# Optimization experiments

Measured on AMD Instinct MI355X. Metric: run time of the kernel, lower is better.

## Reference

```python
import jax, jax.numpy as jnp
import numpy as np

N = 100000      # num nodes
E = 1600000     # num edges
F_IN = 602      # Reddit input features
H = 256         # num_hidden
C = 42          # num_classes


def gcn_conv(x, src, dst, W, b, num_nodes):
    """PyG GCNConv: add self loops, symmetric deg^-1/2 normalization, scatter-add."""
    h = x @ W  # [N, out] dense transform first (PyG order)
    self_idx = jnp.arange(num_nodes, dtype=src.dtype)
    s = jnp.concatenate([src, self_idx])  # [E+N]
    d = jnp.concatenate([dst, self_idx])
    deg = jax.ops.segment_sum(jnp.ones_like(d, dtype=h.dtype), d, num_segments=num_nodes)
    dinv = deg ** -0.5  # deg >= 1 due to self loops
    norm = dinv[s] * dinv[d]  # [E+N]
    msg = h[s] * norm[:, None]  # [E+N, out] gather + scale
    out = jax.ops.segment_sum(msg, d, num_segments=num_nodes)  # scatter-add
    return out + b


def setup_inputs() -> dict:
    key = jax.random.key(0)
    k = jax.random.split(key, 5)
    x = jax.random.normal(k[0], (N, F_IN), dtype=jnp.float32)
    edge_index = jax.random.randint(k[1], (2, E), 0, N, dtype=jnp.int32)
    # Glorot-style init for GCNConv linear weights; bias zeros (PyG default)
    W1 = jax.random.normal(k[2], (F_IN, H), dtype=jnp.float32) * np.float32(1.0 / np.sqrt(F_IN))
    b1 = jnp.zeros((H,), dtype=jnp.float32)
    W2 = jax.random.normal(k[3], (H, C), dtype=jnp.float32) * np.float32(1.0 / np.sqrt(H))
    b2 = jnp.zeros((C,), dtype=jnp.float32)
    return {"x": x, "edge_index": edge_index, "W1": W1, "b1": b1, "W2": W2, "b2": b2}


def reference(x, edge_index, W1, b1, W2, b2):
    src, dst = edge_index[0], edge_index[1]
    num_nodes = x.shape[0]
    h = gcn_conv(x, src, dst, W1, b1, num_nodes)
    h = jax.nn.relu(h)
    # dropout is identity in eval mode (deterministic reference)
    out = gcn_conv(h, src, dst, W2, b2, num_nodes)
    return jax.nn.log_softmax(out, axis=1)
```

## Files before the change

### kernel.cpp

```cpp
#include <hip/hip_runtime.h>
#include <stdint.h>

#define NN 100000
#define NE 1600000
#define FIN 602
#define KP1 608
#define H 256
#define C 42
#define NP2 48
#define NB1 98

typedef __bf16 bf16;
typedef __bf16 bf16x8 __attribute__((ext_vector_type(8)));
typedef float f32x4 __attribute__((ext_vector_type(4)));

__device__ __forceinline__ float b2f(bf16 v) { return (float)v; }
__device__ __forceinline__ bf16 f2b(float v) { return (bf16)v; }
__device__ __forceinline__ float us2f(unsigned short u) {
    union { unsigned int i; float f; } w; w.i = ((unsigned int)u) << 16; return w.f;
}


__global__ void k_zero(int* __restrict__ p, int n) {
    int i = blockIdx.x * 256 + threadIdx.x;
    if (i < n) p[i] = 0;
}

__global__ void k_count(const int* __restrict__ dst, int* __restrict__ cnt) {
    int e = blockIdx.x * 256 + threadIdx.x;
    if (e < NE) atomicAdd(&cnt[dst[e]], 1);
}

__global__ void k_dinv(const int* __restrict__ cnt, float* __restrict__ dinv) {
    int i = blockIdx.x * 256 + threadIdx.x;
    if (i < NN) dinv[i] = rsqrtf((float)(cnt[i] + 1));
}

__global__ __launch_bounds__(256) void k_scan1(const int* __restrict__ cnt,
                                               int* __restrict__ excl, int* __restrict__ bsum) {
    __shared__ int ts[256];
    const int tid = threadIdx.x;
    const int base = blockIdx.x * 1024 + tid * 4;
    int v[4];
#pragma unroll
    for (int j = 0; j < 4; ++j) v[j] = (base + j < NN) ? cnt[base + j] : 0;
    int s = v[0] + v[1] + v[2] + v[3];
    ts[tid] = s;
    __syncthreads();
    for (int off = 1; off < 256; off <<= 1) {
        int t = (tid >= off) ? ts[tid - off] : 0;
        __syncthreads();
        if (tid >= off) ts[tid] += t;
        __syncthreads();
    }
    int prefix = ts[tid] - s;
    if (tid == 255) bsum[blockIdx.x] = ts[255];
    int run = prefix;
#pragma unroll
    for (int j = 0; j < 4; ++j) {
        if (base + j < NN) excl[base + j] = run;
        run += v[j];
    }
}

__global__ __launch_bounds__(128) void k_scan2(int* __restrict__ bsum) {
    __shared__ int ts[128];
    const int tid = threadIdx.x;
    int v = (tid < NB1) ? bsum[tid] : 0;
    ts[tid] = v;
    __syncthreads();
    for (int off = 1; off < 128; off <<= 1) {
        int t = (tid >= off) ? ts[tid - off] : 0;
        __syncthreads();
        if (tid >= off) ts[tid] += t;
        __syncthreads();
    }
    if (tid < NB1) bsum[tid] = ts[tid] - v;
}

__global__ __launch_bounds__(256) void k_scan3(const int* __restrict__ excl, const int* __restrict__ bsum,
                                               int* __restrict__ rowptr, int* __restrict__ cursor) {
    const int tid = threadIdx.x;
    const int base = blockIdx.x * 1024 + tid * 4;
    const int add = bsum[blockIdx.x];
#pragma unroll
    for (int j = 0; j < 4; ++j) {
        int i = base + j;
        if (i < NN) { int r = excl[i] + add; rowptr[i] = r; cursor[i] = r; }
    }
    if (blockIdx.x == 0 && tid == 0) rowptr[NN] = NE;
}

__global__ void k_fill(const int* __restrict__ src, const int* __restrict__ dst,
                       int* __restrict__ cursor, int* __restrict__ esrc) {
    int e = blockIdx.x * 256 + threadIdx.x;
    if (e < NE) {
        int d = dst[e];
        int pos = atomicAdd(&cursor[d], 1);
        esrc[pos] = src[e];
    }
}


__global__ void k_transpose_w1(const float* __restrict__ w1, bf16* __restrict__ w1t) {
    int idx = blockIdx.x * 256 + threadIdx.x;
    int n = idx / KP1;
    int k = idx % KP1;
    w1t[idx] = (k < FIN) ? f2b(w1[(size_t)k * H + n]) : (bf16)0.0f;
}

__global__ void k_transpose_w2(const float* __restrict__ w2, bf16* __restrict__ w2t) {
    int idx = blockIdx.x * 256 + threadIdx.x;
    int n = idx >> 8;
    int k = idx & 255;
    w2t[idx] = (n < C) ? f2b(w2[(size_t)k * C + n]) : (bf16)0.0f;
}


__global__ __launch_bounds__(256) void k_gemm1(const float* __restrict__ x,
                                               const bf16* __restrict__ w1t,
                                               bf16* __restrict__ h1) {
    __shared__ bf16 As[64 * 32];
    const int tid = threadIdx.x;
    const int wave = tid >> 6;
    const int lane = tid & 63;
    const int q = lane >> 4;
    const int r = lane & 15;
    const int row0 = blockIdx.x * 64;

    const int srow = tid >> 2;
    const int sseg = tid & 3;
    int gsrow = row0 + srow;
    if (gsrow >= NN) gsrow = NN - 1;
    const float* xrow = x + (size_t)gsrow * FIN + sseg * 8;

    f32x4 acc[4][4];
#pragma unroll
    for (int a = 0; a < 4; ++a)
#pragma unroll
        for (int b = 0; b < 4; ++b) acc[a][b] = (f32x4){0.f, 0.f, 0.f, 0.f};

    const bf16* bbase = w1t + (size_t)(wave * 64) * KP1;

    for (int kk = 0; kk < 19; ++kk) {
        const int k0 = kk * 32;
        const int c0 = k0 + sseg * 8;
        union { bf16 s[8]; uint4 u; } pk;
        if (c0 + 8 <= FIN) {
            const float2* p = (const float2*)(xrow + k0);
            float2 f0 = p[0], f1 = p[1], f2 = p[2], f3 = p[3];
            pk.s[0] = f2b(f0.x); pk.s[1] = f2b(f0.y);
            pk.s[2] = f2b(f1.x); pk.s[3] = f2b(f1.y);
            pk.s[4] = f2b(f2.x); pk.s[5] = f2b(f2.y);
            pk.s[6] = f2b(f3.x); pk.s[7] = f2b(f3.y);
        } else {
#pragma unroll
            for (int j = 0; j < 8; ++j)
                pk.s[j] = (c0 + j < FIN) ? f2b(xrow[k0 + j]) : (bf16)0.0f;
        }
        __syncthreads();
        *(uint4*)(As + srow * 32 + sseg * 8) = pk.u;
        __syncthreads();

        bf16x8 af[4];
#pragma unroll
        for (int rt = 0; rt < 4; ++rt) {
            union { uint4 u; bf16x8 v; } ua;
            ua.u = *(const uint4*)(As + (rt * 16 + r) * 32 + q * 8);
            af[rt] = ua.v;
        }
#pragma unroll
        for (int ct = 0; ct < 4; ++ct) {
            const bf16* bp = bbase + (size_t)(ct * 16 + r) * KP1 + k0 + q * 8;
            union { uint4 u; bf16x8 v; } ub;
            ub.u = *(const uint4*)bp;
#pragma unroll
            for (int rt = 0; rt < 4; ++rt)
                acc[rt][ct] = __builtin_amdgcn_mfma_f32_16x16x32_bf16(af[rt], ub.v, acc[rt][ct], 0, 0, 0);
        }
    }

#pragma unroll
    for (int rt = 0; rt < 4; ++rt) {
#pragma unroll
        for (int ct = 0; ct < 4; ++ct) {
            const int col = wave * 64 + ct * 16 + r;
#pragma unroll
            for (int rr = 0; rr < 4; ++rr) {
                const int m = row0 + rt * 16 + q * 4 + rr;
                if (m < NN) h1[(size_t)m * H + col] = f2b(acc[rt][ct][rr]);
            }
        }
    }
}


__global__ __launch_bounds__(64) void k_gather1(const int* __restrict__ rowptr,
                                                const int* __restrict__ esrc,
                                                const bf16* __restrict__ h1,
                                                const float* __restrict__ dinv,
                                                const float* __restrict__ b1,
                                                bf16* __restrict__ hb) {
    const int n = blockIdx.x;
    const int tid = threadIdx.x;
    const float dn = dinv[n];

    uint2 u = ((const uint2*)(h1 + (size_t)n * H))[tid];
    float ws = dn * dn;
    float a0 = us2f((unsigned short)(u.x & 0xffff)) * ws;
    float a1 = us2f((unsigned short)(u.x >> 16)) * ws;
    float a2 = us2f((unsigned short)(u.y & 0xffff)) * ws;
    float a3 = us2f((unsigned short)(u.y >> 16)) * ws;

    const int beg = rowptr[n], end = rowptr[n + 1];
    int j = beg;
    for (; j + 3 < end; j += 4) {
        int s0 = esrc[j], s1 = esrc[j + 1], s2 = esrc[j + 2], s3 = esrc[j + 3];
        float w0 = dinv[s0] * dn, w1 = dinv[s1] * dn, w2 = dinv[s2] * dn, w3 = dinv[s3] * dn;
        uint2 v0 = ((const uint2*)(h1 + (size_t)s0 * H))[tid];
        uint2 v1 = ((const uint2*)(h1 + (size_t)s1 * H))[tid];
        uint2 v2 = ((const uint2*)(h1 + (size_t)s2 * H))[tid];
        uint2 v3 = ((const uint2*)(h1 + (size_t)s3 * H))[tid];
        a0 += us2f((unsigned short)(v0.x & 0xffff)) * w0;
        a1 += us2f((unsigned short)(v0.x >> 16)) * w0;
        a2 += us2f((unsigned short)(v0.y & 0xffff)) * w0;
        a3 += us2f((unsigned short)(v0.y >> 16)) * w0;
        a0 += us2f((unsigned short)(v1.x & 0xffff)) * w1;
        a1 += us2f((unsigned short)(v1.x >> 16)) * w1;
        a2 += us2f((unsigned short)(v1.y & 0xffff)) * w1;
        a3 += us2f((unsigned short)(v1.y >> 16)) * w1;
        a0 += us2f((unsigned short)(v2.x & 0xffff)) * w2;
        a1 += us2f((unsigned short)(v2.x >> 16)) * w2;
        a2 += us2f((unsigned short)(v2.y & 0xffff)) * w2;
        a3 += us2f((unsigned short)(v2.y >> 16)) * w2;
        a0 += us2f((unsigned short)(v3.x & 0xffff)) * w3;
        a1 += us2f((unsigned short)(v3.x >> 16)) * w3;
        a2 += us2f((unsigned short)(v3.y & 0xffff)) * w3;
        a3 += us2f((unsigned short)(v3.y >> 16)) * w3;
    }
    for (; j < end; ++j) {
        int s = esrc[j];
        float w = dinv[s] * dn;
        uint2 v = ((const uint2*)(h1 + (size_t)s * H))[tid];
        a0 += us2f((unsigned short)(v.x & 0xffff)) * w;
        a1 += us2f((unsigned short)(v.x >> 16)) * w;
        a2 += us2f((unsigned short)(v.y & 0xffff)) * w;
        a3 += us2f((unsigned short)(v.y >> 16)) * w;
    }

    float4 bb = ((const float4*)b1)[tid];
    a0 += bb.x; a1 += bb.y; a2 += bb.z; a3 += bb.w;
    a0 = a0 > 0.f ? a0 : 0.f;
    a1 = a1 > 0.f ? a1 : 0.f;
    a2 = a2 > 0.f ? a2 : 0.f;
    a3 = a3 > 0.f ? a3 : 0.f;

    union { unsigned short s[4]; uint2 u; } pk;
    union { bf16 b; unsigned short s; } cv;
    cv.b = f2b(a0); pk.s[0] = cv.s;
    cv.b = f2b(a1); pk.s[1] = cv.s;
    cv.b = f2b(a2); pk.s[2] = cv.s;
    cv.b = f2b(a3); pk.s[3] = cv.s;
    ((uint2*)(hb + (size_t)n * H))[tid] = pk.u;
}


__global__ __launch_bounds__(256) void k_gemm2(const bf16* __restrict__ hb,
                                               const bf16* __restrict__ w2t,
                                               bf16* __restrict__ h2) {
    __shared__ bf16 As[256 * 32];
    const int tid = threadIdx.x;
    const int wave = tid >> 6;
    const int lane = tid & 63;
    const int q = lane >> 4;
    const int r = lane & 15;
    const int row0 = blockIdx.x * 256;

    int gsrow = row0 + tid;
    if (gsrow >= NN) gsrow = NN - 1;
    const bf16* arow = hb + (size_t)gsrow * H;

    f32x4 acc[4][3];
#pragma unroll
    for (int a = 0; a < 4; ++a)
#pragma unroll
        for (int b = 0; b < 3; ++b) acc[a][b] = (f32x4){0.f, 0.f, 0.f, 0.f};

    for (int kk = 0; kk < 8; ++kk) {
        const int k0 = kk * 32;
        uint4 c0 = *(const uint4*)(arow + k0);
        uint4 c1 = *(const uint4*)(arow + k0 + 8);
        uint4 c2 = *(const uint4*)(arow + k0 + 16);
        uint4 c3 = *(const uint4*)(arow + k0 + 24);
        __syncthreads();
        uint4* ldst = (uint4*)(As + tid * 32);
        ldst[0] = c0; ldst[1] = c1; ldst[2] = c2; ldst[3] = c3;
        __syncthreads();

        bf16x8 af[4];
#pragma unroll
        for (int rt = 0; rt < 4; ++rt) {
            union { uint4 u; bf16x8 v; } ua;
            ua.u = *(const uint4*)(As + (wave * 64 + rt * 16 + r) * 32 + q * 8);
            af[rt] = ua.v;
        }
#pragma unroll
        for (int ct = 0; ct < 3; ++ct) {
            const bf16* bp = w2t + (size_t)(ct * 16 + r) * H + k0 + q * 8;
            union { uint4 u; bf16x8 v; } ub;
            ub.u = *(const uint4*)bp;
#pragma unroll
            for (int rt = 0; rt < 4; ++rt)
                acc[rt][ct] = __builtin_amdgcn_mfma_f32_16x16x32_bf16(af[rt], ub.v, acc[rt][ct], 0, 0, 0);
        }
    }

#pragma unroll
    for (int rt = 0; rt < 4; ++rt) {
#pragma unroll
        for (int ct = 0; ct < 3; ++ct) {
            const int col = ct * 16 + r;
            if (col < C) {
#pragma unroll
                for (int rr = 0; rr < 4; ++rr) {
                    const int m = row0 + wave * 64 + rt * 16 + q * 4 + rr;
                    if (m < NN) h2[(size_t)m * C + col] = f2b(acc[rt][ct][rr]);
                }
            }
        }
    }
}


__global__ __launch_bounds__(64) void k_gather2(const int* __restrict__ rowptr,
                                                const int* __restrict__ esrc,
                                                const bf16* __restrict__ h2,
                                                const float* __restrict__ dinv,
                                                const float* __restrict__ b2,
                                                float* __restrict__ out) {
    const int n = blockIdx.x;
    const int c = threadIdx.x;
    const float dn = dinv[n];

    float acc = 0.f;
    if (c < C) acc = b2f(h2[(size_t)n * C + c]) * dn * dn;

    const int beg = rowptr[n], end = rowptr[n + 1];
    int j = beg;
    for (; j + 3 < end; j += 4) {
        int s0 = esrc[j], s1 = esrc[j + 1], s2 = esrc[j + 2], s3 = esrc[j + 3];
        float w0 = dinv[s0] * dn, w1 = dinv[s1] * dn, w2 = dinv[s2] * dn, w3 = dinv[s3] * dn;
        if (c < C) {
            float v0 = b2f(h2[(size_t)s0 * C + c]);
            float v1 = b2f(h2[(size_t)s1 * C + c]);
            float v2 = b2f(h2[(size_t)s2 * C + c]);
            float v3 = b2f(h2[(size_t)s3 * C + c]);
            acc += v0 * w0 + v1 * w1 + v2 * w2 + v3 * w3;
        }
    }
    for (; j < end; ++j) {
        int s = esrc[j];
        float w = dinv[s] * dn;
        if (c < C) acc += b2f(h2[(size_t)s * C + c]) * w;
    }

    float v = (c < C) ? acc + b2[c] : -INFINITY;
    float m = v;
#pragma unroll
    for (int o = 32; o > 0; o >>= 1) m = fmaxf(m, __shfl_xor(m, o, 64));
    float ex = (c < C) ? expf(v - m) : 0.f;
    float s = ex;
#pragma unroll
    for (int o = 32; o > 0; o >>= 1) s += __shfl_xor(s, o, 64);
    if (c < C) out[(size_t)n * C + c] = (v - m) - logf(s);
}


extern "C" void kernel_launch(void* const* d_in, const int* in_sizes, int n_in,
                              void* d_out, int out_size, void* d_ws, size_t ws_size,
                              hipStream_t stream) {
    const float* x  = (const float*)d_in[0];
    const int*   ei = (const int*)d_in[1];
    const float* w1 = (const float*)d_in[2];
    const float* b1 = (const float*)d_in[3];
    const float* w2 = (const float*)d_in[4];
    const float* b2 = (const float*)d_in[5];
    float* out = (float*)d_out;

    const int* src = ei;
    const int* dst = ei + NE;

    char* base = (char*)d_ws;
    size_t off = 0;
    auto alloc = [&](size_t bytes) -> void* {
        void* p = base + off;
        off += (bytes + 255) & ~(size_t)255;
        return p;
    };
    int*   cnt    = (int*)alloc((size_t)NN * 4);
    float* dinv   = (float*)alloc((size_t)NN * 4);
    int*   excl   = (int*)alloc((size_t)NN * 4);
    int*   bsum   = (int*)alloc(128 * 4);
    int*   rowptr = (int*)alloc((size_t)(NN + 1) * 4);
    int*   cursor = (int*)alloc((size_t)NN * 4);
    int*   esrc   = (int*)alloc((size_t)NE * 4);
    bf16*  w1t    = (bf16*)alloc((size_t)H * KP1 * 2);
    bf16*  w2t    = (bf16*)alloc((size_t)NP2 * H * 2);
    bf16*  h1     = (bf16*)alloc((size_t)NN * H * 2);
    bf16*  hb     = (bf16*)alloc((size_t)NN * H * 2);
    bf16*  h2     = (bf16*)alloc((size_t)NN * C * 2);
    (void)ws_size;

    k_zero<<<dim3((NN + 255) / 256), dim3(256), 0, stream>>>(cnt, NN);
    k_count<<<dim3((NE + 255) / 256), dim3(256), 0, stream>>>(dst, cnt);
    k_dinv<<<dim3((NN + 255) / 256), dim3(256), 0, stream>>>(cnt, dinv);
    k_scan1<<<dim3(NB1), dim3(256), 0, stream>>>(cnt, excl, bsum);
    k_scan2<<<dim3(1), dim3(128), 0, stream>>>(bsum);
    k_scan3<<<dim3(NB1), dim3(256), 0, stream>>>(excl, bsum, rowptr, cursor);
    k_fill<<<dim3((NE + 255) / 256), dim3(256), 0, stream>>>(src, dst, cursor, esrc);

    k_transpose_w1<<<dim3(KP1), dim3(256), 0, stream>>>(w1, w1t);
    k_transpose_w2<<<dim3(NP2), dim3(256), 0, stream>>>(w2, w2t);

    k_gemm1<<<dim3((NN + 63) / 64), dim3(256), 0, stream>>>(x, w1t, h1);
    k_gather1<<<dim3(NN), dim3(64), 0, stream>>>(rowptr, esrc, h1, dinv, b1, hb);

    k_gemm2<<<dim3((NN + 255) / 256), dim3(256), 0, stream>>>(hb, w2t, h2);
    k_gather2<<<dim3(NN), dim3(64), 0, stream>>>(rowptr, esrc, h2, dinv, b2, out);
}
```

Measured before the change: 796.2 us.

## Double-buffer LDS tiles with register prefetch in both GEMM kernels

Both dense GEMM kernels now prefetch the next A tiles into registers two steps ahead and alternate between two padded LDS buffers, which cuts the barriers per k-step to one. LDS row stride is padded to 40 elements to reduce bank conflicts. k_gemm2 moves to 128-row tiles with more blocks. This is meant to hide global load latency behind MFMA work, at the cost of more registers and LDS per block.

```diff
diff --git a/kernel.cpp b/kernel.cpp
--- a/kernel.cpp
+++ b/kernel.cpp
@@ -9,6 +9,8 @@
 #define C 42
 #define NP2 48
 #define NB1 98
+#define LDA1 40
+#define LDA2 40
 
 typedef __bf16 bf16;
 typedef __bf16 bf16x8 __attribute__((ext_vector_type(8)));
@@ -117,10 +119,60 @@
 }
 
 
+__device__ __forceinline__ void g1_load(const float* xrow, int kk, int sseg, float2 rx[4]) {
+    const int k0 = kk * 32;
+    const int c0 = k0 + sseg * 8;
+    if (c0 + 8 <= FIN) {
+        const float2* p = (const float2*)(xrow + k0);
+        rx[0] = p[0]; rx[1] = p[1]; rx[2] = p[2]; rx[3] = p[3];
+    } else {
+        float t[8];
+#pragma unroll
+        for (int j = 0; j < 8; ++j) t[j] = (c0 + j < FIN) ? xrow[k0 + j] : 0.f;
+        rx[0] = make_float2(t[0], t[1]);
+        rx[1] = make_float2(t[2], t[3]);
+        rx[2] = make_float2(t[4], t[5]);
+        rx[3] = make_float2(t[6], t[7]);
+    }
+}
+
+__device__ __forceinline__ void g1_step(int kk, const float* xrow, float2 rx[4],
+                                        bf16* buf, int srow, int sseg, int q, int r,
+                                        const bf16* bbase, f32x4 acc[4][4], bool prefetch) {
+    union { bf16 s[8]; uint4 u; } pk;
+    pk.s[0] = f2b(rx[0].x); pk.s[1] = f2b(rx[0].y);
+    pk.s[2] = f2b(rx[1].x); pk.s[3] = f2b(rx[1].y);
+    pk.s[4] = f2b(rx[2].x); pk.s[5] = f2b(rx[2].y);
+    pk.s[6] = f2b(rx[3].x); pk.s[7] = f2b(rx[3].y);
+    *(uint4*)(buf + srow * LDA1 + sseg * 8) = pk.u;
+    if (prefetch) g1_load(xrow, kk + 2, sseg, rx);
+    asm volatile("s_waitcnt lgkmcnt(0)" ::: "memory");
+    __builtin_amdgcn_s_barrier();
+
+    const int k0 = kk * 32;
+    bf16x8 af[4];
+#pragma unroll
+    for (int rt = 0; rt < 4; ++rt) {
+        union { uint4 u; bf16x8 v; } ua;
+        ua.u = *(const uint4*)(buf + (rt * 16 + r) * LDA1 + q * 8);
+        af[rt] = ua.v;
+    }
+#pragma unroll
+    for (int ct = 0; ct < 4; ++ct) {
+        const bf16* bp = bbase + (size_t)(ct * 16 + r) * KP1 + k0 + q * 8;
+        union { uint4 u; bf16x8 v; } ub;
+        ub.u = *(const uint4*)bp;
+#pragma unroll
+        for (int rt = 0; rt < 4; ++rt)
+            acc[rt][ct] = __builtin_amdgcn_mfma_f32_16x16x32_bf16(af[rt], ub.v, acc[rt][ct], 0, 0, 0);
+    }
+}
+
 __global__ __launch_bounds__(256) void k_gemm1(const float* __restrict__ x,
                                                const bf16* __restrict__ w1t,
                                                bf16* __restrict__ h1) {
-    __shared__ bf16 As[64 * 32];
+    __shared__ bf16 As0[64 * LDA1];
+    __shared__ bf16 As1[64 * LDA1];
     const int tid = threadIdx.x;
     const int wave = tid >> 6;
     const int lane = tid & 63;
@@ -142,42 +194,15 @@
 
     const bf16* bbase = w1t + (size_t)(wave * 64) * KP1;
 
-    for (int kk = 0; kk < 19; ++kk) {
-        const int k0 = kk * 32;
-        const int c0 = k0 + sseg * 8;
-        union { bf16 s[8]; uint4 u; } pk;
-        if (c0 + 8 <= FIN) {
-            const float2* p = (const float2*)(xrow + k0);
-            float2 f0 = p[0], f1 = p[1], f2 = p[2], f3 = p[3];
-            pk.s[0] = f2b(f0.x); pk.s[1] = f2b(f0.y);
-            pk.s[2] = f2b(f1.x); pk.s[3] = f2b(f1.y);
-            pk.s[4] = f2b(f2.x); pk.s[5] = f2b(f2.y);
-            pk.s[6] = f2b(f3.x); pk.s[7] = f2b(f3.y);
-        } else {
-#pragma unroll
-            for (int j = 0; j < 8; ++j)
-                pk.s[j] = (c0 + j < FIN) ? f2b(xrow[k0 + j]) : (bf16)0.0f;
-        }
-        __syncthreads();
-        *(uint4*)(As + srow * 32 + sseg * 8) = pk.u;
-        __syncthreads();
-
-        bf16x8 af[4];
-#pragma unroll
-        for (int rt = 0; rt < 4; ++rt) {
-            union { uint4 u; bf16x8 v; } ua;
-            ua.u = *(const uint4*)(As + (rt * 16 + r) * 32 + q * 8);
-            af[rt] = ua.v;
-        }
-#pragma unroll
-        for (int ct = 0; ct < 4; ++ct) {
-            const bf16* bp = bbase + (size_t)(ct * 16 + r) * KP1 + k0 + q * 8;
-            union { uint4 u; bf16x8 v; } ub;
-            ub.u = *(const uint4*)bp;
-#pragma unroll
-            for (int rt = 0; rt < 4; ++rt)
-                acc[rt][ct] = __builtin_amdgcn_mfma_f32_16x16x32_bf16(af[rt], ub.v, acc[rt][ct], 0, 0, 0);
-        }
+    float2 ra[4], rb[4];
+    g1_load(xrow, 0, sseg, ra);
+    g1_load(xrow, 1, sseg, rb);
+
+#pragma unroll 1
+    for (int kk = 0; kk < 19; kk += 2) {
+        g1_step(kk, xrow, ra, As0, srow, sseg, q, r, bbase, acc, kk + 2 < 19);
+        if (kk + 1 < 19)
+            g1_step(kk + 1, xrow, rb, As1, srow, sseg, q, r, bbase, acc, kk + 3 < 19);
     }
 
 #pragma unroll
@@ -265,65 +290,83 @@
 }
 
 
+__device__ __forceinline__ void g2_load(const bf16* arow, int kk, uint4 rx[2]) {
+    const bf16* p = arow + kk * 32;
+    rx[0] = *(const uint4*)p;
+    rx[1] = *(const uint4*)(p + 8);
+}
+
+__device__ __forceinline__ void g2_step(int kk, const bf16* arow, uint4 rx[2],
+                                        bf16* buf, int srow, int sseg, int q, int r, int wave,
+                                        const bf16* w2t, f32x4 acc[2][3], bool prefetch) {
+    *(uint4*)(buf + srow * LDA2 + sseg * 16) = rx[0];
+    *(uint4*)(buf + srow * LDA2 + sseg * 16 + 8) = rx[1];
+    if (prefetch) g2_load(arow, kk + 2, rx);
+    asm volatile("s_waitcnt lgkmcnt(0)" ::: "memory");
+    __builtin_amdgcn_s_barrier();
+
+    const int k0 = kk * 32;
+    bf16x8 af[2];
+#pragma unroll
+    for (int rt = 0; rt < 2; ++rt) {
+        union { uint4 u; bf16x8 v; } ua;
+        ua.u = *(const uint4*)(buf + (wave * 32 + rt * 16 + r) * LDA2 + q * 8);
+        af[rt] = ua.v;
+    }
+#pragma unroll
+    for (int ct = 0; ct < 3; ++ct) {
+        const bf16* bp = w2t + (size_t)(ct * 16 + r) * H + k0 + q * 8;
+        union { uint4 u; bf16x8 v; } ub;
+        ub.u = *(const uint4*)bp;
+#pragma unroll
+        for (int rt = 0; rt < 2; ++rt)
+            acc[rt][ct] = __builtin_amdgcn_mfma_f32_16x16x32_bf16(af[rt], ub.v, acc[rt][ct], 0, 0, 0);
+    }
+}
+
 __global__ __launch_bounds__(256) void k_gemm2(const bf16* __restrict__ hb,
                                                const bf16* __restrict__ w2t,
                                                bf16* __restrict__ h2) {
-    __shared__ bf16 As[256 * 32];
+    __shared__ bf16 As0[128 * LDA2];
+    __shared__ bf16 As1[128 * LDA2];
     const int tid = threadIdx.x;
     const int wave = tid >> 6;
     const int lane = tid & 63;
     const int q = lane >> 4;
     const int r = lane & 15;
-    const int row0 = blockIdx.x * 256;
-
-    int gsrow = row0 + tid;
+    const int row0 = blockIdx.x * 128;
+
+    const int srow = tid >> 1;
+    const int sseg = tid & 1;
+    int gsrow = row0 + srow;
     if (gsrow >= NN) gsrow = NN - 1;
-    const bf16* arow = hb + (size_t)gsrow * H;
-
-    f32x4 acc[4][3];
-#pragma unroll
-    for (int a = 0; a < 4; ++a)
+    const bf16* arow = hb + (size_t)gsrow * H + sseg * 16;
+
+    f32x4 acc[2][3];
+#pragma unroll
+    for (int a = 0; a < 2; ++a)
 #pragma unroll
         for (int b = 0; b < 3; ++b) acc[a][b] = (f32x4){0.f, 0.f, 0.f, 0.f};
 
-    for (int kk = 0; kk < 8; ++kk) {
-        const int k0 = kk * 32;
-        uint4 c0 = *(const uint4*)(arow + k0);
-        uint4 c1 = *(const uint4*)(arow + k0 + 8);
-        uint4 c2 = *(const uint4*)(arow + k0 + 16);
-        uint4 c3 = *(const uint4*)(arow + k0 + 24);
-        __syncthreads();
-        uint4* ldst = (uint4*)(As + tid * 32);
-        ldst[0] = c0; ldst[1] = c1; ldst[2] = c2; ldst[3] = c3;
-        __syncthreads();
-
-        bf16x8 af[4];
-#pragma unroll
-        for (int rt = 0; rt < 4; ++rt) {
-            union { uint4 u; bf16x8 v; } ua;
-            ua.u = *(const uint4*)(As + (wave * 64 + rt * 16 + r) * 32 + q * 8);
-            af[rt] = ua.v;
-        }
-#pragma unroll
-        for (int ct = 0; ct < 3; ++ct) {
-            const bf16* bp = w2t + (size_t)(ct * 16 + r) * H + k0 + q * 8;
-            union { uint4 u; bf16x8 v; } ub;
-            ub.u = *(const uint4*)bp;
-#pragma unroll
-            for (int rt = 0; rt < 4; ++rt)
-                acc[rt][ct] = __builtin_amdgcn_mfma_f32_16x16x32_bf16(af[rt], ub.v, acc[rt][ct], 0, 0, 0);
-        }
-    }
-
-#pragma unroll
-    for (int rt = 0; rt < 4; ++rt) {
+    uint4 ra[2], rb[2];
+    g2_load(arow, 0, ra);
+    g2_load(arow, 1, rb);
+
+#pragma unroll 1
+    for (int kk = 0; kk < 8; kk += 2) {
+        g2_step(kk, arow, ra, As0, srow, sseg, q, r, wave, w2t, acc, kk + 2 < 8);
+        g2_step(kk + 1, arow, rb, As1, srow, sseg, q, r, wave, w2t, acc, kk + 3 < 8);
+    }
+
+#pragma unroll
+    for (int rt = 0; rt < 2; ++rt) {
 #pragma unroll
         for (int ct = 0; ct < 3; ++ct) {
             const int col = ct * 16 + r;
             if (col < C) {
 #pragma unroll
                 for (int rr = 0; rr < 4; ++rr) {
-                    const int m = row0 + wave * 64 + rt * 16 + q * 4 + rr;
+                    const int m = row0 + wave * 32 + rt * 16 + q * 4 + rr;
                     if (m < NN) h2[(size_t)m * C + col] = f2b(acc[rt][ct][rr]);
                 }
             }
@@ -425,6 +468,6 @@
     k_gemm1<<<dim3((NN + 63) / 64), dim3(256), 0, stream>>>(x, w1t, h1);
     k_gather1<<<dim3(NN), dim3(64), 0, stream>>>(rowptr, esrc, h1, dinv, b1, hb);
 
-    k_gemm2<<<dim3((NN + 255) / 256), dim3(256), 0, stream>>>(hb, w2t, h2);
+    k_gemm2<<<dim3((NN + 127) / 128), dim3(256), 0, stream>>>(hb, w2t, h2);
     k_gather2<<<dim3(NN), dim3(64), 0, stream>>>(rowptr, esrc, h2, dinv, b2, out);
 }
```

New measurement: 812.9 us. 2.1% more time.

## Load GEMM A fragments directly from global memory, dropping LDS staging and barriers

Applied to the files above, without the earlier changes.

Both dense GEMM kernels now read A-operand fragments straight from global memory into registers instead of staging tiles through shared memory with two barriers per k-step. gemm1 splits the 256 output columns across two blocks per row tile, and gemm2 uses smaller 128-row blocks, to raise block counts. The aim is to remove synchronization stalls and LDS traffic. In exchange, x rows are read redundantly by multiple waves and blocks and the global loads are less coalesced, so cache and bandwidth pressure goes up.

```diff
diff --git a/kernel.cpp b/kernel.cpp
--- a/kernel.cpp
+++ b/kernel.cpp
@@ -120,71 +120,94 @@
 __global__ __launch_bounds__(256) void k_gemm1(const float* __restrict__ x,
                                                const bf16* __restrict__ w1t,
                                                bf16* __restrict__ h1) {
-    __shared__ bf16 As[64 * 32];
     const int tid = threadIdx.x;
     const int wave = tid >> 6;
     const int lane = tid & 63;
     const int q = lane >> 4;
     const int r = lane & 15;
-    const int row0 = blockIdx.x * 64;
-
-    const int srow = tid >> 2;
-    const int sseg = tid & 3;
-    int gsrow = row0 + srow;
-    if (gsrow >= NN) gsrow = NN - 1;
-    const float* xrow = x + (size_t)gsrow * FIN + sseg * 8;
-
-    f32x4 acc[4][4];
+    const int b = blockIdx.x;
+    const int row0 = (b >> 1) * 64;
+    const int col0 = (b & 1) * 128 + wave * 32;
+
+    const float* arow[4];
+#pragma unroll
+    for (int rt = 0; rt < 4; ++rt) {
+        int m = row0 + rt * 16 + r;
+        if (m >= NN) m = NN - 1;
+        arow[rt] = x + (size_t)m * FIN + q * 8;
+    }
+    const bf16* brow[2];
+#pragma unroll
+    for (int ct = 0; ct < 2; ++ct)
+        brow[ct] = w1t + (size_t)(col0 + ct * 16 + r) * KP1 + q * 8;
+
+    f32x4 acc[4][2];
 #pragma unroll
     for (int a = 0; a < 4; ++a)
 #pragma unroll
-        for (int b = 0; b < 4; ++b) acc[a][b] = (f32x4){0.f, 0.f, 0.f, 0.f};
-
-    const bf16* bbase = w1t + (size_t)(wave * 64) * KP1;
-
-    for (int kk = 0; kk < 19; ++kk) {
+        for (int c = 0; c < 2; ++c) acc[a][c] = (f32x4){0.f, 0.f, 0.f, 0.f};
+
+#pragma unroll 2
+    for (int kk = 0; kk < 18; ++kk) {
         const int k0 = kk * 32;
-        const int c0 = k0 + sseg * 8;
-        union { bf16 s[8]; uint4 u; } pk;
-        if (c0 + 8 <= FIN) {
-            const float2* p = (const float2*)(xrow + k0);
+        bf16x8 af[4];
+#pragma unroll
+        for (int rt = 0; rt < 4; ++rt) {
+            const float2* p = (const float2*)(arow[rt] + k0);
             float2 f0 = p[0], f1 = p[1], f2 = p[2], f3 = p[3];
+            union { bf16 s[8]; bf16x8 v; } pk;
             pk.s[0] = f2b(f0.x); pk.s[1] = f2b(f0.y);
             pk.s[2] = f2b(f1.x); pk.s[3] = f2b(f1.y);
             pk.s[4] = f2b(f2.x); pk.s[5] = f2b(f2.y);
             pk.s[6] = f2b(f3.x); pk.s[7] = f2b(f3.y);
-        } else {
-#pragma unroll
-            for (int j = 0; j < 8; ++j)
-                pk.s[j] = (c0 + j < FIN) ? f2b(xrow[k0 + j]) : (bf16)0.0f;
-        }
-        __syncthreads();
-        *(uint4*)(As + srow * 32 + sseg * 8) = pk.u;
-        __syncthreads();
-
-        bf16x8 af[4];
-#pragma unroll
-        for (int rt = 0; rt < 4; ++rt) {
-            union { uint4 u; bf16x8 v; } ua;
-            ua.u = *(const uint4*)(As + (rt * 16 + r) * 32 + q * 8);
-            af[rt] = ua.v;
-        }
-#pragma unroll
-        for (int ct = 0; ct < 4; ++ct) {
-            const bf16* bp = bbase + (size_t)(ct * 16 + r) * KP1 + k0 + q * 8;
+            af[rt] = pk.v;
+        }
+#pragma unroll
+        for (int ct = 0; ct < 2; ++ct) {
             union { uint4 u; bf16x8 v; } ub;
-            ub.u = *(const uint4*)bp;
+            ub.u = *(const uint4*)(brow[ct] + k0);
 #pragma unroll
             for (int rt = 0; rt < 4; ++rt)
                 acc[rt][ct] = __builtin_amdgcn_mfma_f32_16x16x32_bf16(af[rt], ub.v, acc[rt][ct], 0, 0, 0);
         }
     }
 
+    {
+        const int k0 = 576;
+        bf16x8 af[4];
+#pragma unroll
+        for (int rt = 0; rt < 4; ++rt) {
+            union { bf16 s[8]; bf16x8 v; } pk;
+            if (q < 3) {
+                const float2* p = (const float2*)(arow[rt] + k0);
+                float2 f0 = p[0], f1 = p[1], f2 = p[2], f3 = p[3];
+                pk.s[0] = f2b(f0.x); pk.s[1] = f2b(f0.y);
+                pk.s[2] = f2b(f1.x); pk.s[3] = f2b(f1.y);
+                pk.s[4] = f2b(f2.x); pk.s[5] = f2b(f2.y);
+                pk.s[6] = f2b(f3.x); pk.s[7] = f2b(f3.y);
+            } else {
+                const float* p = arow[rt] + k0;
+                pk.s[0] = f2b(p[0]); pk.s[1] = f2b(p[1]);
+#pragma unroll
+                for (int j = 2; j < 8; ++j) pk.s[j] = (bf16)0.0f;
+            }
+            af[rt] = pk.v;
+        }
+#pragma unroll
+        for (int ct = 0; ct < 2; ++ct) {
+            union { uint4 u; bf16x8 v; } ub;
+            ub.u = *(const uint4*)(brow[ct] + k0);
+#pragma unroll
+            for (int rt = 0; rt < 4; ++rt)
+                acc[rt][ct] = __builtin_amdgcn_mfma_f32_16x16x32_bf16(af[rt], ub.v, acc[rt][ct], 0, 0, 0);
+        }
+    }
+
 #pragma unroll
     for (int rt = 0; rt < 4; ++rt) {
 #pragma unroll
-        for (int ct = 0; ct < 4; ++ct) {
-            const int col = wave * 64 + ct * 16 + r;
+        for (int ct = 0; ct < 2; ++ct) {
+            const int col = col0 + ct * 16 + r;
 #pragma unroll
             for (int rr = 0; rr < 4; ++rr) {
                 const int m = row0 + rt * 16 + q * 4 + rr;
@@ -268,62 +291,60 @@
 __global__ __launch_bounds__(256) void k_gemm2(const bf16* __restrict__ hb,
                                                const bf16* __restrict__ w2t,
                                                bf16* __restrict__ h2) {
-    __shared__ bf16 As[256 * 32];
     const int tid = threadIdx.x;
     const int wave = tid >> 6;
     const int lane = tid & 63;
     const int q = lane >> 4;
     const int r = lane & 15;
-    const int row0 = blockIdx.x * 256;
-
-    int gsrow = row0 + tid;
-    if (gsrow >= NN) gsrow = NN - 1;
-    const bf16* arow = hb + (size_t)gsrow * H;
-
-    f32x4 acc[4][3];
-#pragma unroll
-    for (int a = 0; a < 4; ++a)
-#pragma unroll
-        for (int b = 0; b < 3; ++b) acc[a][b] = (f32x4){0.f, 0.f, 0.f, 0.f};
-
+    const int row0 = blockIdx.x * 128 + wave * 32;
+
+    const bf16* arow[2];
+#pragma unroll
+    for (int rt = 0; rt < 2; ++rt) {
+        int m = row0 + rt * 16 + r;
+        if (m >= NN) m = NN - 1;
+        arow[rt] = hb + (size_t)m * H + q * 8;
+    }
+    const bf16* brow[3];
+#pragma unroll
+    for (int ct = 0; ct < 3; ++ct)
+        brow[ct] = w2t + (size_t)(ct * 16 + r) * H + q * 8;
+
+    f32x4 acc[2][3];
+#pragma unroll
+    for (int a = 0; a < 2; ++a)
+#pragma unroll
+        for (int c = 0; c < 3; ++c) acc[a][c] = (f32x4){0.f, 0.f, 0.f, 0.f};
+
+#pragma unroll 2
     for (int kk = 0; kk < 8; ++kk) {
         const int k0 = kk * 32;
-        uint4 c0 = *(const uint4*)(arow + k0);
-        uint4 c1 = *(const uint4*)(arow + k0 + 8);
-        uint4 c2 = *(const uint4*)(arow + k0 + 16);
-        uint4 c3 = *(const uint4*)(arow + k0 + 24);
-        __syncthreads();
-        uint4* ldst = (uint4*)(As + tid * 32);
-        ldst[0] = c0; ldst[1] = c1; ldst[2] = c2; ldst[3] = c3;
-        __syncthreads();
-
-        bf16x8 af[4];
-#pragma unroll
-        for (int rt = 0; rt < 4; ++rt) {
+        bf16x8 af[2];
+#pragma unroll
+        for (int rt = 0; rt < 2; ++rt) {
             union { uint4 u; bf16x8 v; } ua;
-            ua.u = *(const uint4*)(As + (wave * 64 + rt * 16 + r) * 32 + q * 8);
+            ua.u = *(const uint4*)(arow[rt] + k0);
             af[rt] = ua.v;
         }
 #pragma unroll
         for (int ct = 0; ct < 3; ++ct) {
-            const bf16* bp = w2t + (size_t)(ct * 16 + r) * H + k0 + q * 8;
             union { uint4 u; bf16x8 v; } ub;
-            ub.u = *(const uint4*)bp;
-#pragma unroll
-            for (int rt = 0; rt < 4; ++rt)
+            ub.u = *(const uint4*)(brow[ct] + k0);
+#pragma unroll
+            for (int rt = 0; rt < 2; ++rt)
                 acc[rt][ct] = __builtin_amdgcn_mfma_f32_16x16x32_bf16(af[rt], ub.v, acc[rt][ct], 0, 0, 0);
         }
     }
 
 #pragma unroll
-    for (int rt = 0; rt < 4; ++rt) {
+    for (int rt = 0; rt < 2; ++rt) {
 #pragma unroll
         for (int ct = 0; ct < 3; ++ct) {
             const int col = ct * 16 + r;
             if (col < C) {
 #pragma unroll
                 for (int rr = 0; rr < 4; ++rr) {
-                    const int m = row0 + wave * 64 + rt * 16 + q * 4 + rr;
+                    const int m = row0 + rt * 16 + q * 4 + rr;
                     if (m < NN) h2[(size_t)m * C + col] = f2b(acc[rt][ct][rr]);
                 }
             }
@@ -422,9 +443,9 @@
     k_transpose_w1<<<dim3(KP1), dim3(256), 0, stream>>>(w1, w1t);
     k_transpose_w2<<<dim3(NP2), dim3(256), 0, stream>>>(w2, w2t);
 
-    k_gemm1<<<dim3((NN + 63) / 64), dim3(256), 0, stream>>>(x, w1t, h1);
+    k_gemm1<<<dim3(2 * ((NN + 63) / 64)), dim3(256), 0, stream>>>(x, w1t, h1);
     k_gather1<<<dim3(NN), dim3(64), 0, stream>>>(rowptr, esrc, h1, dinv, b1, hb);
 
-    k_gemm2<<<dim3((NN + 255) / 256), dim3(256), 0, stream>>>(hb, w2t, h2);
+    k_gemm2<<<dim3((NN + 127) / 128), dim3(256), 0, stream>>>(hb, w2t, h2);
     k_gather2<<<dim3(NN), dim3(64), 0, stream>>>(rowptr, esrc, h2, dinv, b2, out);
 }
```

Result: slower. 944.3 us (+18.6%).
